# Performance work log

Hardware: AMD Instinct MI355X
Metric: run time of the kernel (lower is better)

The kernel has to match this reference:

```python
import jax, jax.numpy as jnp
import numpy as np

SDE_SIGMA_MIN = 0.01   # VE-SDE sigma(0)
SDE_SIGMA_MAX = 100.0  # VE-SDE sigma(1)
SIGMA_MIN = 1e-4       # model's sigma_min regularizer


def sde_sigma(t):
    # Variance-exploding SDE noise schedule: geometric interpolation.
    return SDE_SIGMA_MIN * (SDE_SIGMA_MAX / SDE_SIGMA_MIN) ** t


def setup_inputs() -> dict:
    key = jax.random.key(0)
    k1, k2, k3 = jax.random.split(key, 3)
    B, N, D = 4096, 8192, 256
    t = jax.random.uniform(k1, (B,), dtype=jnp.float32)          # diffusion times in [0,1)
    x = jax.random.normal(k2, (B, D), dtype=jnp.float32)         # query points
    samples = jax.random.normal(k3, (N, D), dtype=jnp.float32)   # dataset samples
    return {"t": t, "x": x, "samples": samples}


def reference(t, x, samples):
    # t: [B], x: [B, D], samples: [N, D]
    t_scale = sde_sigma(t)                                  # [B]
    denom = (t_scale ** 2 + SIGMA_MIN ** 2)[:, None]        # [B, 1]
    # ||s_i - x_b||^2 via expansion (avoids materializing [B, N, D])
    s2 = jnp.sum(samples ** 2, axis=-1)                     # [N]
    x2 = jnp.sum(x ** 2, axis=-1, keepdims=True)            # [B, 1]
    d2 = x2 - 2.0 * (x @ samples.T) + s2[None, :]           # [B, N]
    # W_i = exp(-0.5 d2 / denom); max-subtract + normalize == stable softmax
    W = jax.nn.softmax(-0.5 * d2 / denom, axis=-1)          # [B, N]
    mean_s = W @ samples                                    # [B, D]
    # t_scale * sum_i W_i (s_i - x) / denom, with sum_i W_i == 1
    return t_scale[:, None] * (mean_s - x) / denom
```

## Files before the change

kernel.cpp:

```cpp
#include <hip/hip_runtime.h>
#include <math.h>


typedef float  f32x4 __attribute__((ext_vector_type(4)));
typedef short  s16x8 __attribute__((ext_vector_type(8)));
typedef unsigned short u16;

#define LOG2E   1.44269504088896f
#define L2_10K  13.2877123795494f
#define L2_001 -6.64385618977472f
#define SMIN2   1e-8f
#define DDIM    256
#define DEFER_THR 12.0f

#if defined(__has_builtin)
#if __has_builtin(__builtin_amdgcn_exp2f)
#define EXP2(x) __builtin_amdgcn_exp2f(x)
#endif
#endif
#ifndef EXP2
#define EXP2(x) exp2f(x)
#endif

#define GL16(gp, lp) \
  __builtin_amdgcn_global_load_lds( \
      (const __attribute__((address_space(1))) unsigned int*)(gp), \
      (__attribute__((address_space(3))) unsigned int*)(lp), 16, 0, 0)

__device__ __forceinline__ u16 bf16_rne(float f) {
  unsigned int u = __builtin_bit_cast(unsigned int, f);
  u = (u + 0x7FFFu + ((u >> 16) & 1u)) >> 16;
  return (u16)u;
}
__device__ __forceinline__ float bf16_to_f(u16 h) {
  unsigned int u = ((unsigned int)h) << 16;
  return __builtin_bit_cast(float, u);
}
__device__ __forceinline__ float f16_to_f(u16 h) {
  int s = (h >> 15) & 1, e = (h >> 10) & 31, m = h & 1023;
  float v;
  if (e == 0)       v = ldexpf((float)m, -24);
  else if (e == 31) v = 3.0e38f;
  else              v = ldexpf((float)(1024 + m), e - 25);
  return s ? -v : v;
}

__device__ __forceinline__ int classify_t_dtype(const void* tp) {
  const u16*          u16p = (const u16*)tp;
  const unsigned int* u32p = (const unsigned int*)tp;
  int c16 = 0, c32 = 0;
  for (int i = 0; i < 128; ++i) {
    u16 u = u16p[i];
    int e = (u >> 7) & 0xFF;
    if (!(u & 0x8000) && e >= 113 && e <= 126) c16++;
  }
  for (int i = 0; i < 64; ++i) {
    unsigned int w = u32p[i];
    int e = (int)((w >> 23) & 0xFF);
    if (!(w & 0x80000000u) && e >= 113 && e <= 126) c32++;
  }
  if (c32 >= 51) return (c16 >= 102) ? 0 : 1;
  return 2;
}
__device__ __forceinline__ float load_t(const void* tp, int i, int mode) {
  float v;
  if (mode == 0)      v = bf16_to_f(((const u16*)tp)[i]);
  else if (mode == 1) v = ((const float*)tp)[i];
  else                v = f16_to_f(((const u16*)tp)[i]);
  return fminf(fmaxf(v, 0.f), 1.f);
}


__global__ __launch_bounds__(256)
void prep_rows(const float* __restrict__ smp, const void* __restrict__ t,
               u16* __restrict__ gkhi, u16* __restrict__ gklo,
               float* __restrict__ gs2, int* __restrict__ tflag, int N)
{
  if (blockIdx.x == 0 && threadIdx.x == 0) *tflag = classify_t_dtype(t);
  int row  = blockIdx.x * 4 + (threadIdx.x >> 6);
  int lane = threadIdx.x & 63;
  float4 v4 = *(const float4*)(smp + (size_t)row * DDIM + lane * 4);
  float v[4] = {v4.x, v4.y, v4.z, v4.w};
  ushort4 h, l;
  u16 hh[4], ll[4];
  float s2 = 0.f;
#pragma unroll
  for (int e = 0; e < 4; ++e) {
    hh[e] = bf16_rne(v[e]);
    ll[e] = bf16_rne(v[e] - bf16_to_f(hh[e]));
    s2 = fmaf(v[e], v[e], s2);
  }
  h.x = hh[0]; h.y = hh[1]; h.z = hh[2]; h.w = hh[3];
  l.x = ll[0]; l.y = ll[1]; l.z = ll[2]; l.w = ll[3];
  int ci  = lane >> 1;
  int col = (((ci ^ (row & 7)) << 3) | ((lane & 1) << 2));
  *(ushort4*)(gkhi + (size_t)row * DDIM + col) = h;
  *(ushort4*)(gklo + (size_t)row * DDIM + col) = l;
#pragma unroll
  for (int msk = 1; msk <= 32; msk <<= 1) s2 += __shfl_xor(s2, msk);
  if (lane == 0) gs2[row] = 0.5f * s2;
}

__global__ __launch_bounds__(256)
void prep_t(const u16* __restrict__ gkhi, u16* __restrict__ gvt, int N)
{
  int d  = threadIdx.x;
  int n0 = blockIdx.x * 32;
  u16 buf[32];
#pragma unroll
  for (int i = 0; i < 32; ++i) {
    int col = ((((d >> 3) ^ (i & 7)) << 3) | (d & 7));
    buf[i] = gkhi[(size_t)(n0 + i) * DDIM + col];
  }
  u16* dst = gvt + ((size_t)blockIdx.x * 256 + d) * 32;
  int vkey = (d >> 1) & 3;
#pragma unroll
  for (int c = 0; c < 4; ++c)
    *(s16x8*)(dst + ((c ^ vkey) << 3)) = *(s16x8*)&buf[c * 8];
}


#define PSTR 40

struct __align__(16) Smem {
  u16 khi[32 * 256];
  u16 klo[32 * 256];
  u16 vt [2][256 * 32];
  u16 p  [4][16 * PSTR];
};

__global__ __launch_bounds__(256, 2)
void flash_kernel(const void* __restrict__ t, const float* __restrict__ x,
                  const u16* __restrict__ gkhi, const u16* __restrict__ gklo,
                  const u16* __restrict__ gvt, const float* __restrict__ gs2,
                  const int* __restrict__ tflag, float* __restrict__ out,
                  float* __restrict__ pO, float* __restrict__ pm,
                  float* __restrict__ pl, int B, int N)
{
  __shared__ Smem sm;
  const int tid  = threadIdx.x;
  const int wave = tid >> 6, lane = tid & 63;
  const int lq = lane >> 4, lr = lane & 15;
  const int m0 = blockIdx.x * 64 + wave * 16;
  const int nsplit = gridDim.y, split = blockIdx.y;
  const int tiles_total = N >> 5;
  const int tq = tiles_total / nsplit, tr = tiles_total % nsplit;
  const int tile0 = split * tq + (split < tr ? split : tr);
  const int iters = tq + (split < tr ? 1 : 0);
  const int n0b = tile0 << 5;
  const int tmode = *tflag;

  float invd[4];
#pragma unroll
  for (int r = 0; r < 4; ++r) {
    int gm = m0 + lq * 4 + r;
    float tv = load_t(t, gm, tmode);
    float ts = EXP2(fmaf(tv, L2_10K, L2_001));
    invd[r] = LOG2E / (ts * ts + SMIN2);
  }

  s16x8 qhi[8], qlo[8];
  {
    const float* xr = x + (size_t)(m0 + lr) * DDIM;
#pragma unroll
    for (int ks = 0; ks < 8; ++ks) {
      const float4* p4 = (const float4*)(xr + ks * 32 + lq * 8);
      float4 a = p4[0], b = p4[1];
      float v[8] = {a.x, a.y, a.z, a.w, b.x, b.y, b.z, b.w};
#pragma unroll
      for (int j = 0; j < 8; ++j) {
        u16 h = bf16_rne(v[j]);
        u16 l = bf16_rne(v[j] - bf16_to_f(h));
        qhi[ks][j] = (short)h;
        qlo[ks][j] = (short)l;
      }
    }
  }

  f32x4 O[16];
#pragma unroll
  for (int dt = 0; dt < 16; ++dt) O[dt] = (f32x4){0.f, 0.f, 0.f, 0.f};
  float mrun[4], lrun[4];
#pragma unroll
  for (int r = 0; r < 4; ++r) { mrun[r] = -1e30f; lrun[r] = 0.f; }

  const int krsw = lr & 7;
  const int wo = (wave << 12) + lane * 16;

  {
    size_t tb = (size_t)n0b << 9;
    const char* gk = (const char*)gkhi + tb + wo;
    const char* gl = (const char*)gklo + tb + wo;
    const char* gv = (const char*)gvt  + tb + wo;
    char* lk = (char*)sm.khi   + (wave << 12);
    char* ll = (char*)sm.klo   + (wave << 12);
    char* lv = (char*)sm.vt[0] + (wave << 12);
    GL16(gk,        lk);        GL16(gk + 1024, lk + 1024);
    GL16(gk + 2048, lk + 2048); GL16(gk + 3072, lk + 3072);
    GL16(gl,        ll);        GL16(gl + 1024, ll + 1024);
    GL16(gl + 2048, ll + 2048); GL16(gl + 3072, ll + 3072);
    GL16(gv,        lv);        GL16(gv + 1024, lv + 1024);
    GL16(gv + 2048, lv + 2048); GL16(gv + 3072, lv + 3072);
  }

  int n0 = n0b, cur = 0;
  for (int it = 0; it < iters; ++it) {
    __syncthreads();

    float s2a = gs2[n0 + lr], s2b = gs2[n0 + 16 + lr];

    f32x4 acc[2];
    acc[0] = (f32x4){0.f, 0.f, 0.f, 0.f};
    acc[1] = (f32x4){0.f, 0.f, 0.f, 0.f};
    __builtin_amdgcn_s_setprio(1);
#pragma unroll
    for (int nt = 0; nt < 2; ++nt) {
#pragma unroll
      for (int ks = 0; ks < 8; ++ks) {
        int co = (((ks << 2) + lq) ^ krsw) << 3;
        const s16x8 bh = *(const s16x8*)&sm.khi[(nt * 16 + lr) * 256 + co];
        const s16x8 bl = *(const s16x8*)&sm.klo[(nt * 16 + lr) * 256 + co];
        acc[nt] = __builtin_amdgcn_mfma_f32_16x16x32_bf16(qhi[ks], bh, acc[nt], 0, 0, 0);
        acc[nt] = __builtin_amdgcn_mfma_f32_16x16x32_bf16(qlo[ks], bh, acc[nt], 0, 0, 0);
        acc[nt] = __builtin_amdgcn_mfma_f32_16x16x32_bf16(qhi[ks], bl, acc[nt], 0, 0, 0);
      }
    }
    __builtin_amdgcn_s_setprio(0);

    __syncthreads();

    if (it + 1 < iters) {
      size_t tb = (size_t)(n0 + 32) << 9;
      const char* gk = (const char*)gkhi + tb + wo;
      const char* gl = (const char*)gklo + tb + wo;
      const char* gv = (const char*)gvt  + tb + wo;
      char* lk = (char*)sm.khi + (wave << 12);
      char* ll = (char*)sm.klo + (wave << 12);
      char* lv = (char*)sm.vt[cur ^ 1] + (wave << 12);
      GL16(gk,        lk);        GL16(gk + 1024, lk + 1024);
      GL16(gk + 2048, lk + 2048); GL16(gk + 3072, lk + 3072);
      GL16(gl,        ll);        GL16(gl + 1024, ll + 1024);
      GL16(gl + 2048, ll + 2048); GL16(gl + 3072, ll + 3072);
      GL16(gv,        lv);        GL16(gv + 1024, lv + 1024);
      GL16(gv + 2048, lv + 2048); GL16(gv + 3072, lv + 3072);
    }

#pragma unroll
    for (int r = 0; r < 4; ++r) {
      float L[2];
      L[0] = (acc[0][r] - s2a) * invd[r];
      L[1] = (acc[1][r] - s2b) * invd[r];
      float tmax = fmaxf(L[0], L[1]);
#pragma unroll
      for (int msk = 1; msk <= 8; msk <<= 1)
        tmax = fmaxf(tmax, __shfl_xor(tmax, msk));
      float mnew = mrun[r];
      if (!__all(tmax - mnew <= DEFER_THR)) {
        mnew = fmaxf(mnew, tmax);
        float alpha = EXP2(mrun[r] - mnew);
        mrun[r] = mnew;
        lrun[r] *= alpha;
#pragma unroll
        for (int dt = 0; dt < 16; ++dt) O[dt][r] *= alpha;
      }
      float ps = 0.f;
#pragma unroll
      for (int nt = 0; nt < 2; ++nt) {
        u16 pq = bf16_rne(EXP2(L[nt] - mnew));
        ps += bf16_to_f(pq);
        sm.p[wave][(lq * 4 + r) * PSTR + nt * 16 + lr] = pq;
      }
#pragma unroll
      for (int msk = 1; msk <= 8; msk <<= 1) ps += __shfl_xor(ps, msk);
      lrun[r] += ps;
    }

    {
      const s16x8 pa = *(const s16x8*)&sm.p[wave][lr * PSTR + lq * 8];
      const u16* vtc = sm.vt[cur];
      __builtin_amdgcn_s_setprio(1);
#pragma unroll
      for (int dt = 0; dt < 16; ++dt) {
        int row = dt * 16 + lr;
        const s16x8 bv = *(const s16x8*)&vtc[(row << 5) + ((lq ^ ((row >> 1) & 3)) << 3)];
        O[dt] = __builtin_amdgcn_mfma_f32_16x16x32_bf16(pa, bv, O[dt], 0, 0, 0);
      }
      __builtin_amdgcn_s_setprio(0);
    }
    cur ^= 1;
    n0 += 32;
  }

  if (nsplit == 1) {
#pragma unroll
    for (int r = 0; r < 4; ++r) {
      int gm = m0 + lq * 4 + r;
      float tv = load_t(t, gm, tmode);
      float ts = EXP2(fmaf(tv, L2_10K, L2_001));
      float den = ts * ts + SMIN2;
      float sc = ts / den;
      float il = 1.f / lrun[r];
#pragma unroll
      for (int dt = 0; dt < 16; ++dt) {
        int d = dt * 16 + lr;
        out[(size_t)gm * DDIM + d] = sc * (O[dt][r] * il - x[(size_t)gm * DDIM + d]);
      }
    }
  } else {
    size_t obase = (size_t)split * B * DDIM;
#pragma unroll
    for (int r = 0; r < 4; ++r) {
      int gm = m0 + lq * 4 + r;
#pragma unroll
      for (int dt = 0; dt < 16; ++dt)
        pO[obase + (size_t)gm * DDIM + dt * 16 + lr] = O[dt][r];
      if (lr == 0) {
        pm[(size_t)split * B + gm] = mrun[r];
        pl[(size_t)split * B + gm] = lrun[r];
      }
    }
  }
}

__global__ __launch_bounds__(256)
void combine_kernel(const void* __restrict__ t, const float* __restrict__ x,
                    const float* __restrict__ pO, const float* __restrict__ pm,
                    const float* __restrict__ pl, float* __restrict__ out,
                    const int* __restrict__ tflag, int nsplit, int B)
{
  int idx = blockIdx.x * 256 + threadIdx.x;
  int b = idx >> 6;
  const int tmode = *tflag;
  float M = -1e30f;
  for (int s = 0; s < nsplit; ++s) M = fmaxf(M, pm[(size_t)s * B + b]);
  float4 num = {0.f, 0.f, 0.f, 0.f};
  float den = 0.f;
  for (int s = 0; s < nsplit; ++s) {
    float w = EXP2(pm[(size_t)s * B + b] - M);
    float4 po = ((const float4*)pO)[(size_t)s * B * 64 + idx];
    num.x += w * po.x; num.y += w * po.y; num.z += w * po.z; num.w += w * po.w;
    den += w * pl[(size_t)s * B + b];
  }
  float il = 1.f / den;
  float tv = load_t(t, b, tmode);
  float ts = EXP2(fmaf(tv, L2_10K, L2_001));
  float sc = ts / (ts * ts + SMIN2);
  float4 xx = ((const float4*)x)[idx];
  float4 o;
  o.x = sc * (num.x * il - xx.x);
  o.y = sc * (num.y * il - xx.y);
  o.z = sc * (num.z * il - xx.z);
  o.w = sc * (num.w * il - xx.w);
  ((float4*)out)[idx] = o;
}

extern "C" void kernel_launch(void* const* d_in, const int* in_sizes, int n_in,
                              void* d_out, int out_size, void* d_ws, size_t ws_size,
                              hipStream_t stream) {
  int xi = 0, si = 0, ti = 0;
  for (int i = 0; i < 3; ++i) {
    if (in_sizes[i] == out_size) xi = i;
    if (in_sizes[i] > in_sizes[si]) si = i;
    if (in_sizes[i] < in_sizes[ti]) ti = i;
  }
  const void*  t   = d_in[ti];
  const float* x   = (const float*)d_in[xi];
  const float* smp = (const float*)d_in[si];
  float* out = (float*)d_out;
  int B = out_size / DDIM;
  int N = in_sizes[si] / DDIM;

  size_t plane = (size_t)N * DDIM;
  u16*   gkhi = (u16*)d_ws;
  u16*   gklo = gkhi + plane;
  u16*   gvt  = gklo + plane;
  float* gs2  = (float*)(gvt + plane);
  int*   tflag = (int*)(gs2 + N);
  float* pO   = gs2 + N + 4;
  size_t fixed = plane * 6 + (size_t)N * 4 + 16;
  size_t per = (size_t)B * DDIM * sizeof(float) + (size_t)B * 2 * sizeof(float);

  const int cand[4] = {8, 4, 2, 1};
  int ns = 1;
  for (int i = 0; i < 4; ++i)
    if (fixed + (size_t)cand[i] * per <= ws_size) { ns = cand[i]; break; }
  float* pm = pO + (size_t)ns * B * DDIM;
  float* pl = pm + (size_t)ns * B;

  prep_rows<<<dim3(N / 4), 256, 0, stream>>>(smp, t, gkhi, gklo, gs2, tflag, N);
  prep_t<<<dim3(N / 32), 256, 0, stream>>>(gkhi, gvt, N);
  flash_kernel<<<dim3(B / 64, ns), 256, 0, stream>>>(t, x, gkhi, gklo, gvt, gs2, tflag,
                                                     out, pO, pm, pl, B, N);
  if (ns > 1)
    combine_kernel<<<dim3(B * 64 / 256), 256, 0, stream>>>(t, x, pO, pm, pl, out, tflag, ns, B);
}
```

Measured before the change: 194.4 us.

## Merge prep kernels, double-buffer K tiles, read V directly from global

The two preprocessing kernels become one launch. The transposed V tile is now built straight from the fp32 samples, so it no longer depends on the swizzled khi buffer. In the flash loop, the V staging buffer in shared memory is dropped, and K hi/lo become double-buffered, with the prefetch issued at the top of each iteration. This removes one __syncthreads per iteration. The PV MFMA operands are now loaded directly from global memory (L2-resident) rather than LDS, which trades LDS traffic and a barrier for global-load latency inside the MFMA loop.

```diff
diff --git a/kernel.cpp b/kernel.cpp
--- a/kernel.cpp
+++ b/kernel.cpp
@@ -70,62 +70,58 @@
   return fminf(fmaxf(v, 0.f), 1.f);
 }
 
-
 __global__ __launch_bounds__(256)
-void prep_rows(const float* __restrict__ smp, const void* __restrict__ t,
-               u16* __restrict__ gkhi, u16* __restrict__ gklo,
-               float* __restrict__ gs2, int* __restrict__ tflag, int N)
+void prep_all(const float* __restrict__ smp, const void* __restrict__ t,
+              u16* __restrict__ gkhi, u16* __restrict__ gklo,
+              float* __restrict__ gs2, u16* __restrict__ gvt,
+              int* __restrict__ tflag, int N)
 {
-  if (blockIdx.x == 0 && threadIdx.x == 0) *tflag = classify_t_dtype(t);
-  int row  = blockIdx.x * 4 + (threadIdx.x >> 6);
-  int lane = threadIdx.x & 63;
-  float4 v4 = *(const float4*)(smp + (size_t)row * DDIM + lane * 4);
-  float v[4] = {v4.x, v4.y, v4.z, v4.w};
-  ushort4 h, l;
-  u16 hh[4], ll[4];
-  float s2 = 0.f;
-#pragma unroll
-  for (int e = 0; e < 4; ++e) {
-    hh[e] = bf16_rne(v[e]);
-    ll[e] = bf16_rne(v[e] - bf16_to_f(hh[e]));
-    s2 = fmaf(v[e], v[e], s2);
-  }
-  h.x = hh[0]; h.y = hh[1]; h.z = hh[2]; h.w = hh[3];
-  l.x = ll[0]; l.y = ll[1]; l.z = ll[2]; l.w = ll[3];
-  int ci  = lane >> 1;
-  int col = (((ci ^ (row & 7)) << 3) | ((lane & 1) << 2));
-  *(ushort4*)(gkhi + (size_t)row * DDIM + col) = h;
-  *(ushort4*)(gklo + (size_t)row * DDIM + col) = l;
-#pragma unroll
-  for (int msk = 1; msk <= 32; msk <<= 1) s2 += __shfl_xor(s2, msk);
-  if (lane == 0) gs2[row] = 0.5f * s2;
-}
-
-__global__ __launch_bounds__(256)
-void prep_t(const u16* __restrict__ gkhi, u16* __restrict__ gvt, int N)
-{
-  int d  = threadIdx.x;
-  int n0 = blockIdx.x * 32;
-  u16 buf[32];
-#pragma unroll
-  for (int i = 0; i < 32; ++i) {
-    int col = ((((d >> 3) ^ (i & 7)) << 3) | (d & 7));
-    buf[i] = gkhi[(size_t)(n0 + i) * DDIM + col];
-  }
-  u16* dst = gvt + ((size_t)blockIdx.x * 256 + d) * 32;
-  int vkey = (d >> 1) & 3;
-#pragma unroll
-  for (int c = 0; c < 4; ++c)
-    *(s16x8*)(dst + ((c ^ vkey) << 3)) = *(s16x8*)&buf[c * 8];
+  int nb_rows = N >> 2;
+  if ((int)blockIdx.x < nb_rows) {
+    if (blockIdx.x == 0 && threadIdx.x == 0) *tflag = classify_t_dtype(t);
+    int row  = blockIdx.x * 4 + (threadIdx.x >> 6);
+    int lane = threadIdx.x & 63;
+    float4 v4 = *(const float4*)(smp + (size_t)row * DDIM + lane * 4);
+    float v[4] = {v4.x, v4.y, v4.z, v4.w};
+    ushort4 h, l;
+    u16 hh[4], ll[4];
+    float s2 = 0.f;
+#pragma unroll
+    for (int e = 0; e < 4; ++e) {
+      hh[e] = bf16_rne(v[e]);
+      ll[e] = bf16_rne(v[e] - bf16_to_f(hh[e]));
+      s2 = fmaf(v[e], v[e], s2);
+    }
+    h.x = hh[0]; h.y = hh[1]; h.z = hh[2]; h.w = hh[3];
+    l.x = ll[0]; l.y = ll[1]; l.z = ll[2]; l.w = ll[3];
+    int ci  = lane >> 1;
+    int col = (((ci ^ (row & 7)) << 3) | ((lane & 1) << 2));
+    *(ushort4*)(gkhi + (size_t)row * DDIM + col) = h;
+    *(ushort4*)(gklo + (size_t)row * DDIM + col) = l;
+#pragma unroll
+    for (int msk = 1; msk <= 32; msk <<= 1) s2 += __shfl_xor(s2, msk);
+    if (lane == 0) gs2[row] = 0.5f * s2;
+  } else {
+    int bt = blockIdx.x - nb_rows;
+    int d  = threadIdx.x;
+    int n0 = bt * 32;
+    u16 buf[32];
+#pragma unroll
+    for (int i = 0; i < 32; ++i)
+      buf[i] = bf16_rne(smp[(size_t)(n0 + i) * DDIM + d]);
+    u16* dst = gvt + ((size_t)bt * 256 + d) * 32;
+#pragma unroll
+    for (int c = 0; c < 4; ++c)
+      *(s16x8*)(dst + c * 8) = *(s16x8*)&buf[c * 8];
+  }
 }
 
 
 #define PSTR 40
 
 struct __align__(16) Smem {
-  u16 khi[32 * 256];
-  u16 klo[32 * 256];
-  u16 vt [2][256 * 32];
+  u16 khi[2][32 * 256];
+  u16 klo[2][32 * 256];
   u16 p  [4][16 * PSTR];
 };
 
@@ -191,24 +187,33 @@
     size_t tb = (size_t)n0b << 9;
     const char* gk = (const char*)gkhi + tb + wo;
     const char* gl = (const char*)gklo + tb + wo;
-    const char* gv = (const char*)gvt  + tb + wo;
-    char* lk = (char*)sm.khi   + (wave << 12);
-    char* ll = (char*)sm.klo   + (wave << 12);
-    char* lv = (char*)sm.vt[0] + (wave << 12);
+    char* lk = (char*)sm.khi[0] + (wave << 12);
+    char* ll = (char*)sm.klo[0] + (wave << 12);
     GL16(gk,        lk);        GL16(gk + 1024, lk + 1024);
     GL16(gk + 2048, lk + 2048); GL16(gk + 3072, lk + 3072);
     GL16(gl,        ll);        GL16(gl + 1024, ll + 1024);
     GL16(gl + 2048, ll + 2048); GL16(gl + 3072, ll + 3072);
-    GL16(gv,        lv);        GL16(gv + 1024, lv + 1024);
-    GL16(gv + 2048, lv + 2048); GL16(gv + 3072, lv + 3072);
   }
 
   int n0 = n0b, cur = 0;
   for (int it = 0; it < iters; ++it) {
     __syncthreads();
 
+    if (it + 1 < iters) {
+      size_t tb = (size_t)(n0 + 32) << 9;
+      const char* gk = (const char*)gkhi + tb + wo;
+      const char* gl = (const char*)gklo + tb + wo;
+      char* lk = (char*)sm.khi[cur ^ 1] + (wave << 12);
+      char* ll = (char*)sm.klo[cur ^ 1] + (wave << 12);
+      GL16(gk,        lk);        GL16(gk + 1024, lk + 1024);
+      GL16(gk + 2048, lk + 2048); GL16(gk + 3072, lk + 3072);
+      GL16(gl,        ll);        GL16(gl + 1024, ll + 1024);
+      GL16(gl + 2048, ll + 2048); GL16(gl + 3072, ll + 3072);
+    }
     float s2a = gs2[n0 + lr], s2b = gs2[n0 + 16 + lr];
 
+    const u16* kbh = sm.khi[cur];
+    const u16* kbl = sm.klo[cur];
     f32x4 acc[2];
     acc[0] = (f32x4){0.f, 0.f, 0.f, 0.f};
     acc[1] = (f32x4){0.f, 0.f, 0.f, 0.f};
@@ -218,32 +223,14 @@
 #pragma unroll
       for (int ks = 0; ks < 8; ++ks) {
         int co = (((ks << 2) + lq) ^ krsw) << 3;
-        const s16x8 bh = *(const s16x8*)&sm.khi[(nt * 16 + lr) * 256 + co];
-        const s16x8 bl = *(const s16x8*)&sm.klo[(nt * 16 + lr) * 256 + co];
+        const s16x8 bh = *(const s16x8*)&kbh[(nt * 16 + lr) * 256 + co];
+        const s16x8 bl = *(const s16x8*)&kbl[(nt * 16 + lr) * 256 + co];
         acc[nt] = __builtin_amdgcn_mfma_f32_16x16x32_bf16(qhi[ks], bh, acc[nt], 0, 0, 0);
         acc[nt] = __builtin_amdgcn_mfma_f32_16x16x32_bf16(qlo[ks], bh, acc[nt], 0, 0, 0);
         acc[nt] = __builtin_amdgcn_mfma_f32_16x16x32_bf16(qhi[ks], bl, acc[nt], 0, 0, 0);
       }
     }
     __builtin_amdgcn_s_setprio(0);
-
-    __syncthreads();
-
-    if (it + 1 < iters) {
-      size_t tb = (size_t)(n0 + 32) << 9;
-      const char* gk = (const char*)gkhi + tb + wo;
-      const char* gl = (const char*)gklo + tb + wo;
-      const char* gv = (const char*)gvt  + tb + wo;
-      char* lk = (char*)sm.khi + (wave << 12);
-      char* ll = (char*)sm.klo + (wave << 12);
-      char* lv = (char*)sm.vt[cur ^ 1] + (wave << 12);
-      GL16(gk,        lk);        GL16(gk + 1024, lk + 1024);
-      GL16(gk + 2048, lk + 2048); GL16(gk + 3072, lk + 3072);
-      GL16(gl,        ll);        GL16(gl + 1024, ll + 1024);
-      GL16(gl + 2048, ll + 2048); GL16(gl + 3072, ll + 3072);
-      GL16(gv,        lv);        GL16(gv + 1024, lv + 1024);
-      GL16(gv + 2048, lv + 2048); GL16(gv + 3072, lv + 3072);
-    }
 
 #pragma unroll
     for (int r = 0; r < 4; ++r) {
@@ -277,12 +264,12 @@
 
     {
       const s16x8 pa = *(const s16x8*)&sm.p[wave][lr * PSTR + lq * 8];
-      const u16* vtc = sm.vt[cur];
+      const u16* gvb = gvt + (size_t)(n0 >> 5) * 8192;
       __builtin_amdgcn_s_setprio(1);
 #pragma unroll
       for (int dt = 0; dt < 16; ++dt) {
         int row = dt * 16 + lr;
-        const s16x8 bv = *(const s16x8*)&vtc[(row << 5) + ((lq ^ ((row >> 1) & 3)) << 3)];
+        const s16x8 bv = *(const s16x8*)&gvb[row * 32 + lq * 8];
         O[dt] = __builtin_amdgcn_mfma_f32_16x16x32_bf16(pa, bv, O[dt], 0, 0, 0);
       }
       __builtin_amdgcn_s_setprio(0);
@@ -387,8 +374,8 @@
   float* pm = pO + (size_t)ns * B * DDIM;
   float* pl = pm + (size_t)ns * B;
 
-  prep_rows<<<dim3(N / 4), 256, 0, stream>>>(smp, t, gkhi, gklo, gs2, tflag, N);
-  prep_t<<<dim3(N / 32), 256, 0, stream>>>(gkhi, gvt, N);
+  prep_all<<<dim3(N / 4 + N / 32), 256, 0, stream>>>(smp, t, gkhi, gklo, gs2,
+                                                     gvt, tflag, N);
   flash_kernel<<<dim3(B / 64, ns), 256, 0, stream>>>(t, x, gkhi, gklo, gvt, gs2, tflag,
                                                      out, pO, pm, pl, B, N);
   if (ns > 1)
```

Result: slower. 219.2 us (+12.7%).

## Transpose QK MFMA to keep P in registers and merge prep kernels

Applied to the files above, without the earlier changes.

Swaps the MFMA operands in the QK^T product so the score tile comes out transposed. Each lane then owns a single query row, which cuts the per-row max/sum shuffle reductions. The P matrix is rebuilt into the PV MFMA's A-operand layout with cross-lane shuffles instead of a round trip through shared memory. The two prep kernels are merged into one launch, and the V-transpose branch now reads directly from the fp32 samples instead of depending on the hi plane. The cost is extra shuffles and selects per tile, plus an uncoalesced strided read pattern in the transpose branch.

```diff
diff --git a/kernel.cpp b/kernel.cpp
--- a/kernel.cpp
+++ b/kernel.cpp
@@ -4,6 +4,7 @@
 
 typedef float  f32x4 __attribute__((ext_vector_type(4)));
 typedef short  s16x8 __attribute__((ext_vector_type(8)));
+typedef unsigned int u32x4 __attribute__((ext_vector_type(4)));
 typedef unsigned short u16;
 
 #define LOG2E   1.44269504088896f
@@ -70,63 +71,58 @@
   return fminf(fmaxf(v, 0.f), 1.f);
 }
 
-
 __global__ __launch_bounds__(256)
-void prep_rows(const float* __restrict__ smp, const void* __restrict__ t,
-               u16* __restrict__ gkhi, u16* __restrict__ gklo,
-               float* __restrict__ gs2, int* __restrict__ tflag, int N)
+void prep_all(const float* __restrict__ smp, const void* __restrict__ t,
+              u16* __restrict__ gkhi, u16* __restrict__ gklo,
+              float* __restrict__ gs2, u16* __restrict__ gvt,
+              int* __restrict__ tflag, int N)
 {
-  if (blockIdx.x == 0 && threadIdx.x == 0) *tflag = classify_t_dtype(t);
-  int row  = blockIdx.x * 4 + (threadIdx.x >> 6);
-  int lane = threadIdx.x & 63;
-  float4 v4 = *(const float4*)(smp + (size_t)row * DDIM + lane * 4);
-  float v[4] = {v4.x, v4.y, v4.z, v4.w};
-  ushort4 h, l;
-  u16 hh[4], ll[4];
-  float s2 = 0.f;
-#pragma unroll
-  for (int e = 0; e < 4; ++e) {
-    hh[e] = bf16_rne(v[e]);
-    ll[e] = bf16_rne(v[e] - bf16_to_f(hh[e]));
-    s2 = fmaf(v[e], v[e], s2);
-  }
-  h.x = hh[0]; h.y = hh[1]; h.z = hh[2]; h.w = hh[3];
-  l.x = ll[0]; l.y = ll[1]; l.z = ll[2]; l.w = ll[3];
-  int ci  = lane >> 1;
-  int col = (((ci ^ (row & 7)) << 3) | ((lane & 1) << 2));
-  *(ushort4*)(gkhi + (size_t)row * DDIM + col) = h;
-  *(ushort4*)(gklo + (size_t)row * DDIM + col) = l;
-#pragma unroll
-  for (int msk = 1; msk <= 32; msk <<= 1) s2 += __shfl_xor(s2, msk);
-  if (lane == 0) gs2[row] = 0.5f * s2;
-}
-
-__global__ __launch_bounds__(256)
-void prep_t(const u16* __restrict__ gkhi, u16* __restrict__ gvt, int N)
-{
-  int d  = threadIdx.x;
-  int n0 = blockIdx.x * 32;
-  u16 buf[32];
-#pragma unroll
-  for (int i = 0; i < 32; ++i) {
-    int col = ((((d >> 3) ^ (i & 7)) << 3) | (d & 7));
-    buf[i] = gkhi[(size_t)(n0 + i) * DDIM + col];
-  }
-  u16* dst = gvt + ((size_t)blockIdx.x * 256 + d) * 32;
-  int vkey = (d >> 1) & 3;
-#pragma unroll
-  for (int c = 0; c < 4; ++c)
-    *(s16x8*)(dst + ((c ^ vkey) << 3)) = *(s16x8*)&buf[c * 8];
-}
-
-
-#define PSTR 40
+  int nb_rows = N >> 2;
+  if ((int)blockIdx.x < nb_rows) {
+    if (blockIdx.x == 0 && threadIdx.x == 0) *tflag = classify_t_dtype(t);
+    int row  = blockIdx.x * 4 + (threadIdx.x >> 6);
+    int lane = threadIdx.x & 63;
+    float4 v4 = *(const float4*)(smp + (size_t)row * DDIM + lane * 4);
+    float v[4] = {v4.x, v4.y, v4.z, v4.w};
+    ushort4 h, l;
+    u16 hh[4], ll[4];
+    float s2 = 0.f;
+#pragma unroll
+    for (int e = 0; e < 4; ++e) {
+      hh[e] = bf16_rne(v[e]);
+      ll[e] = bf16_rne(v[e] - bf16_to_f(hh[e]));
+      s2 = fmaf(v[e], v[e], s2);
+    }
+    h.x = hh[0]; h.y = hh[1]; h.z = hh[2]; h.w = hh[3];
+    l.x = ll[0]; l.y = ll[1]; l.z = ll[2]; l.w = ll[3];
+    int ci  = lane >> 1;
+    int col = (((ci ^ (row & 7)) << 3) | ((lane & 1) << 2));
+    *(ushort4*)(gkhi + (size_t)row * DDIM + col) = h;
+    *(ushort4*)(gklo + (size_t)row * DDIM + col) = l;
+#pragma unroll
+    for (int msk = 1; msk <= 32; msk <<= 1) s2 += __shfl_xor(s2, msk);
+    if (lane == 0) gs2[row] = 0.5f * s2;
+  } else {
+    int bt = blockIdx.x - nb_rows;
+    int d  = threadIdx.x;
+    int n0 = bt * 32;
+    u16 buf[32];
+#pragma unroll
+    for (int i = 0; i < 32; ++i)
+      buf[i] = bf16_rne(smp[(size_t)(n0 + i) * DDIM + d]);
+    u16* dst = gvt + ((size_t)bt * 256 + d) * 32;
+    int vkey = (d >> 1) & 3;
+#pragma unroll
+    for (int c = 0; c < 4; ++c)
+      *(s16x8*)(dst + ((c ^ vkey) << 3)) = *(s16x8*)&buf[c * 8];
+  }
+}
+
 
 struct __align__(16) Smem {
   u16 khi[32 * 256];
   u16 klo[32 * 256];
   u16 vt [2][256 * 32];
-  u16 p  [4][16 * PSTR];
 };
 
 __global__ __launch_bounds__(256, 2)
@@ -150,13 +146,11 @@
   const int n0b = tile0 << 5;
   const int tmode = *tflag;
 
-  float invd[4];
-#pragma unroll
-  for (int r = 0; r < 4; ++r) {
-    int gm = m0 + lq * 4 + r;
-    float tv = load_t(t, gm, tmode);
+  float invd;
+  {
+    float tv = load_t(t, m0 + lr, tmode);
     float ts = EXP2(fmaf(tv, L2_10K, L2_001));
-    invd[r] = LOG2E / (ts * ts + SMIN2);
+    invd = LOG2E / (ts * ts + SMIN2);
   }
 
   s16x8 qhi[8], qlo[8];
@@ -180,12 +174,11 @@
   f32x4 O[16];
 #pragma unroll
   for (int dt = 0; dt < 16; ++dt) O[dt] = (f32x4){0.f, 0.f, 0.f, 0.f};
-  float mrun[4], lrun[4];
-#pragma unroll
-  for (int r = 0; r < 4; ++r) { mrun[r] = -1e30f; lrun[r] = 0.f; }
+  float mrun = -1e30f, lrun = 0.f;
 
   const int krsw = lr & 7;
   const int wo = (wave << 12) + lane * 16;
+  const int lq4 = lq << 2;
 
   {
     size_t tb = (size_t)n0b << 9;
@@ -207,7 +200,8 @@
   for (int it = 0; it < iters; ++it) {
     __syncthreads();
 
-    float s2a = gs2[n0 + lr], s2b = gs2[n0 + 16 + lr];
+    float4 s2a4 = *(const float4*)(gs2 + n0 + lq4);
+    float4 s2b4 = *(const float4*)(gs2 + n0 + 16 + lq4);
 
     f32x4 acc[2];
     acc[0] = (f32x4){0.f, 0.f, 0.f, 0.f};
@@ -220,9 +214,9 @@
         int co = (((ks << 2) + lq) ^ krsw) << 3;
         const s16x8 bh = *(const s16x8*)&sm.khi[(nt * 16 + lr) * 256 + co];
         const s16x8 bl = *(const s16x8*)&sm.klo[(nt * 16 + lr) * 256 + co];
-        acc[nt] = __builtin_amdgcn_mfma_f32_16x16x32_bf16(qhi[ks], bh, acc[nt], 0, 0, 0);
-        acc[nt] = __builtin_amdgcn_mfma_f32_16x16x32_bf16(qlo[ks], bh, acc[nt], 0, 0, 0);
-        acc[nt] = __builtin_amdgcn_mfma_f32_16x16x32_bf16(qhi[ks], bl, acc[nt], 0, 0, 0);
+        acc[nt] = __builtin_amdgcn_mfma_f32_16x16x32_bf16(bh, qhi[ks], acc[nt], 0, 0, 0);
+        acc[nt] = __builtin_amdgcn_mfma_f32_16x16x32_bf16(bh, qlo[ks], acc[nt], 0, 0, 0);
+        acc[nt] = __builtin_amdgcn_mfma_f32_16x16x32_bf16(bl, qhi[ks], acc[nt], 0, 0, 0);
       }
     }
     __builtin_amdgcn_s_setprio(0);
@@ -245,38 +239,66 @@
       GL16(gv + 2048, lv + 2048); GL16(gv + 3072, lv + 3072);
     }
 
+    float L0[4], L1[4];
+    float tmax = -1e30f;
 #pragma unroll
     for (int r = 0; r < 4; ++r) {
-      float L[2];
-      L[0] = (acc[0][r] - s2a) * invd[r];
-      L[1] = (acc[1][r] - s2b) * invd[r];
-      float tmax = fmaxf(L[0], L[1]);
-#pragma unroll
-      for (int msk = 1; msk <= 8; msk <<= 1)
-        tmax = fmaxf(tmax, __shfl_xor(tmax, msk));
-      float mnew = mrun[r];
-      if (!__all(tmax - mnew <= DEFER_THR)) {
-        mnew = fmaxf(mnew, tmax);
-        float alpha = EXP2(mrun[r] - mnew);
-        mrun[r] = mnew;
-        lrun[r] *= alpha;
-#pragma unroll
-        for (int dt = 0; dt < 16; ++dt) O[dt][r] *= alpha;
+      L0[r] = (acc[0][r] - s2a4[r]) * invd;
+      L1[r] = (acc[1][r] - s2b4[r]) * invd;
+      tmax = fmaxf(tmax, fmaxf(L0[r], L1[r]));
+    }
+    tmax = fmaxf(tmax, __shfl_xor(tmax, 16));
+    tmax = fmaxf(tmax, __shfl_xor(tmax, 32));
+    float mnew = mrun;
+    if (!__all(tmax - mnew <= DEFER_THR)) {
+      mnew = fmaxf(mrun, tmax);
+      float alpha = EXP2(mrun - mnew);
+      mrun = mnew;
+      lrun *= alpha;
+      float a0 = __shfl(alpha, lq4 + 0), a1 = __shfl(alpha, lq4 + 1);
+      float a2 = __shfl(alpha, lq4 + 2), a3 = __shfl(alpha, lq4 + 3);
+#pragma unroll
+      for (int dt = 0; dt < 16; ++dt) {
+        O[dt][0] *= a0; O[dt][1] *= a1; O[dt][2] *= a2; O[dt][3] *= a3;
       }
-      float ps = 0.f;
-#pragma unroll
-      for (int nt = 0; nt < 2; ++nt) {
-        u16 pq = bf16_rne(EXP2(L[nt] - mnew));
-        ps += bf16_to_f(pq);
-        sm.p[wave][(lq * 4 + r) * PSTR + nt * 16 + lr] = pq;
-      }
-#pragma unroll
-      for (int msk = 1; msk <= 8; msk <<= 1) ps += __shfl_xor(ps, msk);
-      lrun[r] += ps;
-    }
-
+    }
+    u16 p0[4], p1[4];
+    float ps = 0.f;
+#pragma unroll
+    for (int r = 0; r < 4; ++r) {
+      p0[r] = bf16_rne(EXP2(L0[r] - mnew));
+      p1[r] = bf16_rne(EXP2(L1[r] - mnew));
+      ps += bf16_to_f(p0[r]) + bf16_to_f(p1[r]);
+    }
+    ps += __shfl_xor(ps, 16);
+    ps += __shfl_xor(ps, 32);
+    lrun += ps;
+
+    s16x8 pa;
     {
-      const s16x8 pa = *(const s16x8*)&sm.p[wave][lr * PSTR + lq * 8];
+      unsigned A0 = (unsigned)p0[0] | ((unsigned)p0[1] << 16);
+      unsigned A1 = (unsigned)p0[2] | ((unsigned)p0[3] << 16);
+      unsigned B0 = (unsigned)p1[0] | ((unsigned)p1[1] << 16);
+      unsigned B1 = (unsigned)p1[2] | ((unsigned)p1[3] << 16);
+      int s0 = ((lq & 1) << 5) + lr;
+      int s1 = s0 + 16;
+      unsigned xa0 = (unsigned)__shfl((int)A0, s0);
+      unsigned xa1 = (unsigned)__shfl((int)A1, s0);
+      unsigned xa2 = (unsigned)__shfl((int)A0, s1);
+      unsigned xa3 = (unsigned)__shfl((int)A1, s1);
+      unsigned xb0 = (unsigned)__shfl((int)B0, s0);
+      unsigned xb1 = (unsigned)__shfl((int)B1, s0);
+      unsigned xb2 = (unsigned)__shfl((int)B0, s1);
+      unsigned xb3 = (unsigned)__shfl((int)B1, s1);
+      u32x4 pw;
+      pw.x = (lq < 2) ? xa0 : xb0;
+      pw.y = (lq < 2) ? xa1 : xb1;
+      pw.z = (lq < 2) ? xa2 : xb2;
+      pw.w = (lq < 2) ? xa3 : xb3;
+      pa = __builtin_bit_cast(s16x8, pw);
+    }
+
+    {
       const u16* vtc = sm.vt[cur];
       __builtin_amdgcn_s_setprio(1);
 #pragma unroll
@@ -292,32 +314,35 @@
   }
 
   if (nsplit == 1) {
+    float inv = 1.f / lrun;
+    float il0 = __shfl(inv, lq4 + 0), il1 = __shfl(inv, lq4 + 1);
+    float il2 = __shfl(inv, lq4 + 2), il3 = __shfl(inv, lq4 + 3);
+    float il[4] = {il0, il1, il2, il3};
 #pragma unroll
     for (int r = 0; r < 4; ++r) {
-      int gm = m0 + lq * 4 + r;
+      int gm = m0 + lq4 + r;
       float tv = load_t(t, gm, tmode);
       float ts = EXP2(fmaf(tv, L2_10K, L2_001));
       float den = ts * ts + SMIN2;
       float sc = ts / den;
-      float il = 1.f / lrun[r];
 #pragma unroll
       for (int dt = 0; dt < 16; ++dt) {
         int d = dt * 16 + lr;
-        out[(size_t)gm * DDIM + d] = sc * (O[dt][r] * il - x[(size_t)gm * DDIM + d]);
+        out[(size_t)gm * DDIM + d] = sc * (O[dt][r] * il[r] - x[(size_t)gm * DDIM + d]);
       }
     }
   } else {
     size_t obase = (size_t)split * B * DDIM;
 #pragma unroll
     for (int r = 0; r < 4; ++r) {
-      int gm = m0 + lq * 4 + r;
+      int gm = m0 + lq4 + r;
 #pragma unroll
       for (int dt = 0; dt < 16; ++dt)
         pO[obase + (size_t)gm * DDIM + dt * 16 + lr] = O[dt][r];
-      if (lr == 0) {
-        pm[(size_t)split * B + gm] = mrun[r];
-        pl[(size_t)split * B + gm] = lrun[r];
-      }
+    }
+    if (lane < 16) {
+      pm[(size_t)split * B + m0 + lane] = mrun;
+      pl[(size_t)split * B + m0 + lane] = lrun;
     }
   }
 }
@@ -387,8 +412,8 @@
   float* pm = pO + (size_t)ns * B * DDIM;
   float* pl = pm + (size_t)ns * B;
 
-  prep_rows<<<dim3(N / 4), 256, 0, stream>>>(smp, t, gkhi, gklo, gs2, tflag, N);
-  prep_t<<<dim3(N / 32), 256, 0, stream>>>(gkhi, gvt, N);
+  prep_all<<<dim3(N / 4 + N / 32), 256, 0, stream>>>(smp, t, gkhi, gklo, gs2,
+                                                     gvt, tflag, N);
   flash_kernel<<<dim3(B / 64, ns), 256, 0, stream>>>(t, x, gkhi, gklo, gvt, gs2, tflag,
                                                      out, pO, pm, pl, B, N);
   if (ns > 1)
```

Result: faster. 167.6 us (median of 2 runs) (-13.8%).
